# Performance work log

Measured on AMD Instinct MI355X. Metric: run time of the kernel, lower is better.

Reference implementation:

```python
import jax, jax.numpy as jnp
import numpy as np

FREQ_DIM = 32
TIME_DIM = 32
HEADS = 8
TWO_PI = 6.283185307179586


def get_embeddings(B, H, W, freq_dim, time_dim, dtype):
    # freq embeddings over the height (frequency) axis
    nf = freq_dim // 2
    ln_x = jnp.log2(jnp.arange(0, H * nf, dtype=jnp.float32))
    ln_x = ln_x.at[0].set(-2.0)
    ln_x = ln_x.reshape(H, nf).T  # [nf, H]
    ln_x = ln_x * jnp.arange(1, nf + 1, dtype=jnp.float32)[:, None]
    # view_as_real(exp(1j*theta)) -> (cos, sin), interleaved per order along channel dim
    freq = jnp.stack([jnp.cos(ln_x), jnp.sin(ln_x)], axis=1).reshape(freq_dim, H)  # [freq_dim, H]
    freq = jnp.broadcast_to(freq[None, :, :, None], (B, freq_dim, H, W))

    # time embeddings over the width (time) axis
    nt = time_dim // 2
    k = jnp.arange(0, nt, dtype=jnp.float32) + 0.5  # [nt]
    x = jnp.arange(0, nt * W, dtype=jnp.float32).reshape(W, nt).T  # [nt, W]
    theta = k[:, None] * x / (W * nt) * TWO_PI  # [nt, W]
    time = jnp.stack([jnp.cos(theta), jnp.sin(theta)], axis=1).reshape(time_dim, W)  # [time_dim, W]
    time = jnp.broadcast_to(time[None, :, None, :], (B, time_dim, H, W))

    return jnp.concatenate([freq, time], axis=1).astype(dtype)  # [B, freq_dim+time_dim, H, W]


def setup_inputs() -> dict:
    key = jax.random.key(0)
    ks = jax.random.split(key, 6)
    B, C, H, W = 2, 512, 64, 32
    qkC = C + FREQ_DIM + TIME_DIM  # 576
    inner = HEADS * 64  # 512
    return {
        "hidden_states": jax.random.normal(ks[0], (B, C, H, W), dtype=jnp.float32),
        "Wq": jax.random.normal(ks[1], (qkC, inner), dtype=jnp.float32) * 0.02,
        "Wk": jax.random.normal(ks[2], (qkC, inner), dtype=jnp.float32) * 0.02,
        "Wv": jax.random.normal(ks[3], (C, inner), dtype=jnp.float32) * 0.02,
        "Wout": jax.random.normal(ks[4], (inner, C), dtype=jnp.float32) * 0.02,
        "bout": jnp.zeros((C,), dtype=jnp.float32),
    }


def reference(hidden_states, Wq, Wk, Wv, Wout, bout):
    B, C, H, W = hidden_states.shape
    emb = get_embeddings(B, H, W, FREQ_DIM, TIME_DIM, hidden_states.dtype)
    qk_hs = jnp.concatenate([hidden_states, emb], axis=1)  # [B, qkC, H, W]

    S = H * W
    qk_hs = qk_hs.reshape(B, -1, S).transpose(0, 2, 1)  # [B, S, qkC]
    v_hs = hidden_states.reshape(B, C, S).transpose(0, 2, 1)  # [B, S, C]

    q = qk_hs @ Wq  # [B, S, inner]
    k = qk_hs @ Wk
    v = v_hs @ Wv

    hd_qk = q.shape[-1] // HEADS
    hd_v = v.shape[-1] // HEADS
    q = q.reshape(B, S, HEADS, hd_qk).transpose(0, 2, 1, 3)  # [B, h, S, d]
    k = k.reshape(B, S, HEADS, hd_qk).transpose(0, 2, 1, 3)
    v = v.reshape(B, S, HEADS, hd_v).transpose(0, 2, 1, 3)

    scale = 1.0 / jnp.sqrt(jnp.asarray(hd_qk, dtype=q.dtype))
    scores = jnp.einsum('bhqd,bhkd->bhqk', q, k) * scale
    attn = jax.nn.softmax(scores, axis=-1)
    o = jnp.einsum('bhqk,bhkd->bhqd', attn, v)  # [B, h, S, d_v]

    o = o.transpose(0, 2, 1, 3).reshape(B, S, HEADS * hd_v)
    o = o @ Wout + bout  # [B, S, C]
    o = o.transpose(0, 2, 1).reshape(B, C, H, W)

    return o + hidden_states  # residual_connection=True, rescale_output_factor=1.0
```

## Files before the change

kernel.cpp:

```cpp
#include <hip/hip_runtime.h>
#include <math.h>

#define B_    2
#define C_    512
#define H_    64
#define W_    32
#define S_    2048
#define QKC_  576
#define INNER_ 512
#define NH_   8
#define HD_   64
#define TWO_PI_ 6.283185307179586f

typedef __attribute__((ext_vector_type(8))) short bfrag;
typedef __attribute__((ext_vector_type(4))) float ffrag;
typedef __attribute__((ext_vector_type(16))) float f16v;

typedef __attribute__((address_space(1))) const unsigned int as1_u32;
typedef __attribute__((address_space(3))) unsigned int as3_u32;

__device__ __forceinline__ ushort f2bf(float f) {
    unsigned u = __builtin_bit_cast(unsigned, f);
    unsigned r = (u + 0x7FFFu + ((u >> 16) & 1u)) >> 16;
    return (ushort)r;
}

__device__ __forceinline__ f16v zero16() {
    f16v z;
    #pragma unroll
    for (int i = 0; i < 16; i++) z[i] = 0.f;
    return z;
}

#define GLD(gp_, lp_) __builtin_amdgcn_global_load_lds((as1_u32*)(gp_), (as3_u32*)(lp_), 16, 0, 0)
#define EXPA(dst_, x_) asm("v_exp_f32 %0, %1" : "=v"(dst_) : "v"(x_))
#define SC_LOG2E 0.18033688011f

__global__ void k_trans_emb(const float* __restrict__ hid, ushort* __restrict__ X) {
    __shared__ float t[32][33];
    int b  = blockIdx.z;
    int s0 = blockIdx.x * 32, c0 = blockIdx.y * 32;
    int tx = threadIdx.x, ty = threadIdx.y;
    if (c0 < 512) {
        t[ty][tx] = hid[((size_t)b * C_ + (c0 + ty)) * S_ + s0 + tx];
        __syncthreads();
        X[((size_t)(b * S_ + s0 + ty)) * QKC_ + c0 + tx] = f2bf(t[tx][ty]);
    } else {
        int c = c0 - 512 + tx;
        int s = s0 + ty;
        int h = s >> 5, w = s & 31;
        float val;
        if (c < 32) {
            int f = c >> 1;
            int n = h * 16 + f;
            float lx = (n == 0) ? -2.0f : log2f((float)n);
            float arg = lx * (float)(f + 1);
            val = (c & 1) ? sinf(arg) : cosf(arg);
        } else {
            int tt = (c - 32) >> 1;
            float theta = ((float)tt + 0.5f) * (float)(w * 16 + tt) * (TWO_PI_ / 512.0f);
            val = (c & 1) ? sinf(theta) : cosf(theta);
        }
        X[(size_t)(b * S_ + s) * QKC_ + c0 + tx] = f2bf(val);
    }
}

__global__ void k_wtrans_all(const float* __restrict__ Wq, const float* __restrict__ Wk,
                             const float* __restrict__ Wv, const float* __restrict__ Wo,
                             ushort* __restrict__ Wqt, ushort* __restrict__ Wkt,
                             ushort* __restrict__ Wvt, ushort* __restrict__ Wot) {
    __shared__ float t[32][33];
    int z = blockIdx.z;
    const float* W; ushort* Wt; int K;
    if (z == 0)      { W = Wq; Wt = Wqt; K = QKC_; }
    else if (z == 1) { W = Wk; Wt = Wkt; K = QKC_; }
    else if (z == 2) { W = Wv; Wt = Wvt; K = C_; }
    else             { W = Wo; Wt = Wot; K = INNER_; }
    int k0 = blockIdx.x * 32, n0 = blockIdx.y * 32;
    if (k0 >= K) return;
    int tx = threadIdx.x, ty = threadIdx.y;
    t[ty][tx] = W[(size_t)(k0 + ty) * 512 + n0 + tx];
    __syncthreads();
    Wt[(size_t)(n0 + ty) * K + k0 + tx] = f2bf(t[tx][ty]);
}

#define GSTAGE(buf_, k0_) {                                                   \
    _Pragma("unroll")                                                         \
    for (int i_ = 0; i_ < 6; i_++)                                            \
        GLD(gp[i_] + (k0_), tl + (buf_) * 12288 + lo[i_]); }

__global__ __launch_bounds__(256, 3) void k_qkv(const ushort* __restrict__ X,
                                                const ushort* __restrict__ Wqt,
                                                const ushort* __restrict__ Wkt,
                                                const ushort* __restrict__ Wvt,
                                                ushort* __restrict__ Qb,
                                                ushort* __restrict__ Kpk,
                                                ushort* __restrict__ Vpk) {
    __shared__ ushort __attribute__((aligned(16))) tl[2 * 12288];

    int tid = threadIdx.x;
    int l = tid & 63, wv = tid >> 6;
    int wr = wv >> 1, wc = wv & 1;
    int bid = blockIdx.x;
    int lgc = (bid & 7) * 96 + (bid >> 3);
    int bx = lgc % 24, by = lgc / 24;
    int n0 = bx * 64, m0 = by * 128;
    int sel = n0 >> 9, n0l = n0 & 511;
    const ushort* Bt = (sel == 0) ? Wqt : (sel == 1) ? Wkt : Wvt;
    const int K = (sel < 2) ? QKC_ : C_;
    const int nst = K >> 6;
    int l15 = l & 15, lg = l >> 4;
    int swz = l15 & 7;

    const ushort* gp[6];
    unsigned lo[6];
    {
        int rsub = l >> 3;
        int clog = (l & 7) ^ rsub;
        #pragma unroll
        for (int i = 0; i < 6; i++) {
            int c = wv * 6 + i;
            lo[i] = c * 512;
            if (c < 16) gp[i] = X  + (size_t)(m0  + c * 8        + rsub) * QKC_ + clog * 8;
            else        gp[i] = Bt + (size_t)(n0l + (c - 16) * 8 + rsub) * K    + clog * 8;
        }
    }

    ffrag acc[4][2];
    #pragma unroll
    for (int i = 0; i < 4; i++)
        #pragma unroll
        for (int j = 0; j < 2; j++) acc[i][j] = (ffrag){0.f, 0.f, 0.f, 0.f};

    GSTAGE(0, 0);
    int cur = 0;
    for (int kt = 0; kt < nst; kt++) {
        __syncthreads();
        if (kt + 1 < nst) GSTAGE(cur ^ 1, (kt + 1) * 64);
        const ushort* As = tl + cur * 12288;
        const ushort* Bs = As + 8192;
        #pragma unroll
        for (int ks = 0; ks < 2; ks++) {
            int cl = ks * 4 + lg;
            int ch = (cl ^ swz) * 8;
            bfrag af[4], bf[2];
            #pragma unroll
            for (int mi = 0; mi < 4; mi++)
                af[mi] = *(const bfrag*)(As + (wr * 64 + mi * 16 + l15) * 64 + ch);
            #pragma unroll
            for (int nj = 0; nj < 2; nj++)
                bf[nj] = *(const bfrag*)(Bs + (wc * 32 + nj * 16 + l15) * 64 + ch);
            #pragma unroll
            for (int mi = 0; mi < 4; mi++)
                #pragma unroll
                for (int nj = 0; nj < 2; nj++)
                    acc[mi][nj] = __builtin_amdgcn_mfma_f32_16x16x32_bf16(af[mi], bf[nj], acc[mi][nj], 0, 0, 0);
        }
        cur ^= 1;
    }

    if (sel == 0) {
        #pragma unroll
        for (int mi = 0; mi < 4; mi++)
            #pragma unroll
            for (int nj = 0; nj < 2; nj++)
                #pragma unroll
                for (int r = 0; r < 4; r++) {
                    int row = m0 + wr * 64 + mi * 16 + lg * 4 + r;
                    int col = n0l + wc * 32 + nj * 16 + l15;
                    Qb[(size_t)row * INNER_ + col] = f2bf(acc[mi][nj][r]);
                }
    } else {
        ushort (*Ct)[136] = (ushort(*)[136])tl;
        __syncthreads();
        #pragma unroll
        for (int mi = 0; mi < 4; mi++)
            #pragma unroll
            for (int nj = 0; nj < 2; nj++)
                #pragma unroll
                for (int r = 0; r < 4; r++)
                    Ct[wc * 32 + nj * 16 + l15][wr * 64 + mi * 16 + lg * 4 + r] = f2bf(acc[mi][nj][r]);
        __syncthreads();
        int pair = (m0 >> 11) * 8 + (n0l >> 6);
        int kvb0 = (m0 & 2047) >> 5;
        if (sel == 1) {
            #pragma unroll
            for (int p = 0; p < 4; p++) {
                int cid = tid + p * 256;
                int sl = cid >> 7, kv = cid & 127;
                bfrag tmp;
                #pragma unroll
                for (int j = 0; j < 8; j++) tmp[j] = (short)Ct[sl * 8 + j][kv];
                ushort* dst = Kpk + ((size_t)((pair * 64 + kvb0 + (kv >> 5)) * 8 + sl)) * 256 + (kv & 31) * 8;
                *(uint4*)dst = __builtin_bit_cast(uint4, tmp);
            }
        } else {
            #pragma unroll
            for (int p = 0; p < 4; p++) {
                int cid = tid + p * 256;
                int d = cid >> 4, mc = cid & 15;
                uint4 v = *(uint4*)&Ct[d][mc * 8];
                ushort* dst = Vpk + ((size_t)((pair * 64 + kvb0 + (mc >> 2)) * 4 + (mc & 3))) * 512 + d * 8;
                *(uint4*)dst = v;
            }
        }
    }
}

__global__ __launch_bounds__(256, 2) void k_og(const ushort* __restrict__ Ob,
                                               const ushort* __restrict__ Wot,
                                               const float* __restrict__ bias,
                                               const float* __restrict__ hid,
                                               float* __restrict__ out) {
    __shared__ ushort __attribute__((aligned(16))) tl[2 * 12288];

    int tid = threadIdx.x;
    int l = tid & 63, wv = tid >> 6;
    int wr = wv >> 1, wc = wv & 1;
    int bid = blockIdx.x;
    int lgc = (bid & 7) * 32 + (bid >> 3);
    int bx = lgc & 7, by = lgc >> 3;
    int n0 = bx * 64, m0 = by * 128;
    int l15 = l & 15, lg = l >> 4;
    int swz = l15 & 7;

    const ushort* gp[6];
    unsigned lo[6];
    {
        int rsub = l >> 3;
        int clog = (l & 7) ^ rsub;
        #pragma unroll
        for (int i = 0; i < 6; i++) {
            int c = wv * 6 + i;
            lo[i] = c * 512;
            if (c < 16) gp[i] = Ob  + (size_t)(m0 + c * 8        + rsub) * INNER_ + clog * 8;
            else        gp[i] = Wot + (size_t)(n0 + (c - 16) * 8 + rsub) * INNER_ + clog * 8;
        }
    }

    ffrag acc[4][2];
    #pragma unroll
    for (int i = 0; i < 4; i++)
        #pragma unroll
        for (int j = 0; j < 2; j++) acc[i][j] = (ffrag){0.f, 0.f, 0.f, 0.f};

    GSTAGE(0, 0);
    int cur = 0;
    for (int kt = 0; kt < 8; kt++) {
        __syncthreads();
        if (kt < 7) GSTAGE(cur ^ 1, (kt + 1) * 64);
        const ushort* As = tl + cur * 12288;
        const ushort* Bs = As + 8192;
        #pragma unroll
        for (int ks = 0; ks < 2; ks++) {
            int cl = ks * 4 + lg;
            int ch = (cl ^ swz) * 8;
            bfrag af[4], bf[2];
            #pragma unroll
            for (int mi = 0; mi < 4; mi++)
                af[mi] = *(const bfrag*)(As + (wr * 64 + mi * 16 + l15) * 64 + ch);
            #pragma unroll
            for (int nj = 0; nj < 2; nj++)
                bf[nj] = *(const bfrag*)(Bs + (wc * 32 + nj * 16 + l15) * 64 + ch);
            #pragma unroll
            for (int mi = 0; mi < 4; mi++)
                #pragma unroll
                for (int nj = 0; nj < 2; nj++)
                    acc[mi][nj] = __builtin_amdgcn_mfma_f32_16x16x32_bf16(af[mi], bf[nj], acc[mi][nj], 0, 0, 0);
        }
        cur ^= 1;
    }

    float (*Cf)[129] = (float(*)[129])tl;
    float bv[2];
    #pragma unroll
    for (int nj = 0; nj < 2; nj++) bv[nj] = bias[n0 + wc * 32 + nj * 16 + l15];
    __syncthreads();
    #pragma unroll
    for (int mi = 0; mi < 4; mi++)
        #pragma unroll
        for (int nj = 0; nj < 2; nj++)
            #pragma unroll
            for (int r = 0; r < 4; r++)
                Cf[wc * 32 + nj * 16 + l15][wr * 64 + mi * 16 + lg * 4 + r] = acc[mi][nj][r] + bv[nj];
    __syncthreads();
    int b = m0 >> 11, s0m = m0 & 2047;
    #pragma unroll
    for (int p = 0; p < 8; p++) {
        int f = p * 256 + tid;
        int c = f >> 5, sq = (f & 31) * 4;
        size_t o = (((size_t)(b * 512 + n0 + c)) << 11) + s0m + sq;
        float4 hv = *(const float4*)(hid + o);
        float4 cv = *(float4*)&Cf[c][sq];
        cv.x += hv.x; cv.y += hv.y; cv.z += hv.z; cv.w += hv.w;
        *(float4*)(out + o) = cv;
    }
}

#define CVTPK(dst, a, b) asm("v_cvt_pk_bf16_f32 %0, %1, %2" : "=v"(dst) : "v"(a), "v"(b))
#define SWAP32(a, b)     asm("v_permlane32_swap_b32 %0, %1" : "+v"(a), "+v"(b))

#define ASTAGE(buf_, kt_) {                                                   \
    const ushort* g_ = (qg ? vpb : kpb) + (size_t)(kt_) * 2048 + l * 8;       \
    ushort* lp_ = ktv + spb + (buf_) * 4096 + (qg ? 2048 : 0);                \
    _Pragma("unroll")                                                         \
    for (int i_ = 0; i_ < 4; i_++)                                            \
        GLD(g_ + i_ * 512, lp_ + i_ * 512); }

__global__ __launch_bounds__(512, 4) void k_attn(const ushort* __restrict__ Qf,
                                                 const ushort* __restrict__ Kpk,
                                                 const ushort* __restrict__ Vpk,
                                                 ushort* __restrict__ Ob) {
    __shared__ __attribute__((aligned(16))) char smem[69632];
    ushort* ktv = (ushort*)smem;
    float*  cmb = (float*)smem;
    float*  mlsh = (float*)(smem + 67584);

    const int id = blockIdx.x;
    const int lgc = (id & 7) * 64 + (id >> 3);
    const int qb = lgc & 31, pair = lgc >> 5;
    const int hd = pair & 7, b = pair >> 3;

    const int tid = threadIdx.x;
    const int l = tid & 63, wv = tid >> 6;
    const int qg = wv >> 2, sp = wv & 3;
    const int l31 = l & 31, hi = l >> 5;
    const int hoff = hd * HD_;
    const int brow = b * S_ + qb * 64;

    bfrag qf[4];
    {
        const ushort* qp = Qf + (size_t)(brow + qg * 32 + l31) * INNER_ + hoff + hi * 8;
        #pragma unroll
        for (int ks = 0; ks < 4; ks++) qf[ks] = *(const bfrag*)(qp + ks * 16);
    }

    const ushort* kpb = Kpk + ((size_t)pair * 64 + sp * 16) * 2048;
    const ushort* vpb = Vpk + ((size_t)pair * 64 + sp * 16) * 2048;
    const int spb  = sp * 8192;
    const int koff = l31 * 8 + hi * 256;
    const int voff = l31 * 8 + hi * 512;

    ASTAGE(0, 0);

    float m_run = -INFINITY, l_run = 0.f;
    f16v acc0 = zero16(), acc1 = zero16();
    int buf = 0;

    for (int kt = 0; kt < 16; kt++) {
        __syncthreads();
        if (kt < 15) ASTAGE(buf ^ 1, kt + 1);

        const ushort* Kt = ktv + spb + buf * 4096;
        const ushort* Vt = Kt + 2048;

        f16v sf0 = zero16();
        #pragma unroll
        for (int ks = 0; ks < 4; ks++) {
            bfrag kfr = *(const bfrag*)(Kt + ks * 512 + koff);
            sf0 = __builtin_amdgcn_mfma_f32_32x32x16_bf16(kfr, qf[ks], sf0, 0, 0, 0);
        }

        float t8[8];
        #pragma unroll
        for (int j = 0; j < 8; j++) t8[j] = fmaxf(sf0[j], sf0[j + 8]);
        float t4a = fmaxf(t8[0], t8[4]), t4b = fmaxf(t8[1], t8[5]);
        float t4c = fmaxf(t8[2], t8[6]), t4d = fmaxf(t8[3], t8[7]);
        float tm = fmaxf(fmaxf(t4a, t4b), fmaxf(t4c, t4d));
        tm = fmaxf(tm, __shfl_xor(tm, 32));
        if (!__all(tm <= m_run + 64.0f)) {
            float mn = fmaxf(m_run, tm);
            float corr; EXPA(corr, (m_run - mn) * SC_LOG2E);
            l_run *= corr;
            #pragma unroll
            for (int j = 0; j < 16; j++) { acc0[j] *= corr; acc1[j] *= corr; }
            m_run = mn;
        }
        float nm = -m_run * SC_LOG2E;
        #pragma unroll
        for (int j = 0; j < 16; j++) { float p; EXPA(p, fmaf(sf0[j], SC_LOG2E, nm)); sf0[j] = p; }
        float s8[8];
        #pragma unroll
        for (int j = 0; j < 8; j++) s8[j] = sf0[j] + sf0[j + 8];
        float ls = ((s8[0] + s8[4]) + (s8[1] + s8[5])) + ((s8[2] + s8[6]) + (s8[3] + s8[7]));
        ls += __shfl_xor(ls, 32);
        l_run += ls;

        #pragma unroll
        for (int s = 0; s < 2; s++) {
            unsigned A0, B0, A1, B1;
            CVTPK(A0, sf0[s * 8 + 0], sf0[s * 8 + 1]); CVTPK(B0, sf0[s * 8 + 4], sf0[s * 8 + 5]);
            SWAP32(A0, B0);
            CVTPK(A1, sf0[s * 8 + 2], sf0[s * 8 + 3]); CVTPK(B1, sf0[s * 8 + 6], sf0[s * 8 + 7]);
            SWAP32(A1, B1);
            uint4 u; u.x = A0; u.y = A1; u.z = B0; u.w = B1;
            bfrag pa = __builtin_bit_cast(bfrag, u);
            bfrag v0 = *(const bfrag*)(Vt + s * 1024 + voff);
            bfrag v1 = *(const bfrag*)(Vt + s * 1024 + voff + 256);
            acc0 = __builtin_amdgcn_mfma_f32_32x32x16_bf16(v0, pa, acc0, 0, 0, 0);
            acc1 = __builtin_amdgcn_mfma_f32_32x32x16_bf16(v1, pa, acc1, 0, 0, 0);
        }

        buf ^= 1;
    }

    if (hi == 0) {
        mlsh[(qg * 4 + sp) * 64 + l31]      = m_run;
        mlsh[(qg * 4 + sp) * 64 + 32 + l31] = l_run;
    }
    __syncthreads();
    {
        float* creg = cmb + (qg * 4 + sp) * 2112;
        #pragma unroll
        for (int j = 0; j < 16; j++) {
            int d0 = (j & 3) + 8 * (j >> 2) + 4 * hi;
            creg[d0 * 33 + l31]        = acc0[j];
            creg[(d0 + 32) * 33 + l31] = acc1[j];
        }
    }
    __syncthreads();
    {
        int qgE = tid >> 8;
        int t2 = tid & 255;
        int qq = t2 >> 3, cc = t2 & 7;
        float mh[4], lh[4], cs[4];
        float mg = -INFINITY;
        #pragma unroll
        for (int h = 0; h < 4; h++) {
            mh[h] = mlsh[(qgE * 4 + h) * 64 + qq];
            lh[h] = mlsh[(qgE * 4 + h) * 64 + 32 + qq];
            mg = fmaxf(mg, mh[h]);
        }
        float tot = 0.f;
        #pragma unroll
        for (int h = 0; h < 4; h++) { EXPA(cs[h], (mh[h] - mg) * SC_LOG2E); tot += cs[h] * lh[h]; }
        float inv = 1.0f / tot;
        bfrag ov;
        #pragma unroll
        for (int j = 0; j < 8; j++) {
            int d = cc * 8 + j;
            float s = 0.f;
            #pragma unroll
            for (int h = 0; h < 4; h++) s += cs[h] * cmb[(qgE * 4 + h) * 2112 + d * 33 + qq];
            ov[j] = (short)f2bf(s * inv);
        }
        *(uint4*)(Ob + (size_t)(brow + qgE * 32 + qq) * INNER_ + hoff + cc * 8) = __builtin_bit_cast(uint4, ov);
    }
}

extern "C" void kernel_launch(void* const* d_in, const int* in_sizes, int n_in,
                              void* d_out, int out_size, void* d_ws, size_t ws_size,
                              hipStream_t stream) {
    const float* hid  = (const float*)d_in[0];
    const float* Wq   = (const float*)d_in[1];
    const float* Wk   = (const float*)d_in[2];
    const float* Wv   = (const float*)d_in[3];
    const float* Wout = (const float*)d_in[4];
    const float* bout = (const float*)d_in[5];
    float* out = (float*)d_out;

    const int M = B_ * S_;
    char* w = (char*)d_ws;
    ushort* X    = (ushort*)w;                    w += (size_t)M * QKC_ * 2;
    ushort* Qb   = (ushort*)w;                    w += (size_t)M * INNER_ * 2;
    ushort* Kpk  = (ushort*)w;                    w += (size_t)M * INNER_ * 2;
    ushort* Vpk  = (ushort*)w;                    w += (size_t)M * INNER_ * 2;
    ushort* Ob   = (ushort*)w;                    w += (size_t)M * INNER_ * 2;
    ushort* Wqt  = (ushort*)w;                    w += (size_t)INNER_ * QKC_ * 2;
    ushort* Wkt  = (ushort*)w;                    w += (size_t)INNER_ * QKC_ * 2;
    ushort* Wvt  = (ushort*)w;                    w += (size_t)INNER_ * C_ * 2;
    ushort* Wot  = (ushort*)w;                    w += (size_t)C_ * INNER_ * 2;

    k_wtrans_all<<<dim3(18, 16, 4), dim3(32, 32), 0, stream>>>(Wq, Wk, Wv, Wout,
                                                               Wqt, Wkt, Wvt, Wot);
    k_trans_emb<<<dim3(S_ / 32, 18, B_), dim3(32, 32), 0, stream>>>(hid, X);

    k_qkv<<<dim3(768), 256, 0, stream>>>(X, Wqt, Wkt, Wvt, Qb, Kpk, Vpk);

    k_attn<<<dim3(512), 512, 0, stream>>>(Qb, Kpk, Vpk, Ob);

    k_og<<<dim3(256), 256, 0, stream>>>(Ob, Wot, bout, hid, out);
}
```

Before: 66.80 us.

## Restructure attention with per-wave private K/V staging and 128-row query tiles

Attention blocks now cover 128 query rows with 8 waves, arranged as 4 query groups by 2 key splits, and the grid halves to 256 blocks. Each wave streams its own K and V tiles into a private double-buffered LDS region, synchronised with waitcnt instead of block-wide barriers. MFMA sections are wrapped in s_setprio, and the XCD-aware block mapping is changed. This removes per-iteration __syncthreads, but it uses twice the shared memory, lowers blocks per CU, halves the split-K parallelism, and gives fewer blocks to fill 256 CUs.

Result: slower. 72.83 us (+9.0%).

```diff
diff --git a/kernel.cpp b/kernel.cpp
--- a/kernel.cpp
+++ b/kernel.cpp
@@ -301,43 +301,46 @@
 #define SWAP32(a, b)     asm("v_permlane32_swap_b32 %0, %1" : "+v"(a), "+v"(b))
 
 #define ASTAGE(buf_, kt_) {                                                   \
-    const ushort* g_ = (qg ? vpb : kpb) + (size_t)(kt_) * 2048 + l * 8;       \
-    ushort* lp_ = ktv + spb + (buf_) * 4096 + (qg ? 2048 : 0);                \
+    const ushort* gk_ = kpb + (size_t)(kt_) * 2048 + l * 8;                   \
+    const ushort* gv_ = vpb + (size_t)(kt_) * 2048 + l * 8;                   \
+    ushort* lk_ = lbase + (buf_) * 4096;                                      \
     _Pragma("unroll")                                                         \
-    for (int i_ = 0; i_ < 4; i_++)                                            \
-        GLD(g_ + i_ * 512, lp_ + i_ * 512); }
-
-__global__ __launch_bounds__(512, 4) void k_attn(const ushort* __restrict__ Qf,
+    for (int i_ = 0; i_ < 4; i_++) GLD(gk_ + i_ * 512, lk_ + i_ * 512);       \
+    _Pragma("unroll")                                                         \
+    for (int i_ = 0; i_ < 4; i_++) GLD(gv_ + i_ * 512, lk_ + 2048 + i_ * 512); }
+
+__global__ __launch_bounds__(512, 2) void k_attn(const ushort* __restrict__ Qf,
                                                  const ushort* __restrict__ Kpk,
                                                  const ushort* __restrict__ Vpk,
                                                  ushort* __restrict__ Ob) {
-    __shared__ __attribute__((aligned(16))) char smem[69632];
-    ushort* ktv = (ushort*)smem;
-    float*  cmb = (float*)smem;
-    float*  mlsh = (float*)(smem + 67584);
-
-    const int id = blockIdx.x;
-    const int lgc = (id & 7) * 64 + (id >> 3);
-    const int qb = lgc & 31, pair = lgc >> 5;
+    __shared__ __attribute__((aligned(16))) char smem[133120];
+    ushort* ktv  = (ushort*)smem;
+    float*  cmb  = (float*)smem;
+    float*  mlsh = (float*)(smem + 131072);
+
+    const int id  = blockIdx.x;
+    const int xcd = id & 7, wi = id >> 3;
+    const int pair = xcd * 2 + (wi >> 4);
+    const int qt   = wi & 15;
     const int hd = pair & 7, b = pair >> 3;
 
     const int tid = threadIdx.x;
-    const int l = tid & 63, wv = tid >> 6;
-    const int qg = wv >> 2, sp = wv & 3;
+    const int l = tid & 63, wvid = tid >> 6;
+    const int qi = wvid >> 1, sp = wvid & 1;
     const int l31 = l & 31, hi = l >> 5;
     const int hoff = hd * HD_;
-    const int brow = b * S_ + qb * 64;
+    const int brow = b * S_ + qt * 128;
 
     bfrag qf[4];
     {
-        const ushort* qp = Qf + (size_t)(brow + qg * 32 + l31) * INNER_ + hoff + hi * 8;
+        const ushort* qp = Qf + (size_t)(brow + qi * 32 + l31) * INNER_ + hoff + hi * 8;
         #pragma unroll
         for (int ks = 0; ks < 4; ks++) qf[ks] = *(const bfrag*)(qp + ks * 16);
     }
 
-    const ushort* kpb = Kpk + ((size_t)pair * 64 + sp * 16) * 2048;
-    const ushort* vpb = Vpk + ((size_t)pair * 64 + sp * 16) * 2048;
-    const int spb  = sp * 8192;
+    const ushort* kpb = Kpk + ((size_t)pair * 64 + sp * 32) * 2048;
+    const ushort* vpb = Vpk + ((size_t)pair * 64 + sp * 32) * 2048;
+    ushort* lbase = ktv + wvid * 8192;
     const int koff = l31 * 8 + hi * 256;
     const int voff = l31 * 8 + hi * 512;
 
@@ -347,19 +350,27 @@
     f16v acc0 = zero16(), acc1 = zero16();
     int buf = 0;
 
-    for (int kt = 0; kt < 16; kt++) {
-        __syncthreads();
-        if (kt < 15) ASTAGE(buf ^ 1, kt + 1);
-
-        const ushort* Kt = ktv + spb + buf * 4096;
+    for (int kt = 0; kt < 32; kt++) {
+        if (kt < 31) {
+            asm volatile("s_waitcnt lgkmcnt(0)" ::: "memory");
+            ASTAGE(buf ^ 1, kt + 1);
+            asm volatile("s_waitcnt vmcnt(8)" ::: "memory");
+        } else {
+            asm volatile("s_waitcnt vmcnt(0)" ::: "memory");
+        }
+        __builtin_amdgcn_sched_barrier(0);
+
+        const ushort* Kt = lbase + buf * 4096;
         const ushort* Vt = Kt + 2048;
 
         f16v sf0 = zero16();
+        __builtin_amdgcn_s_setprio(1);
         #pragma unroll
         for (int ks = 0; ks < 4; ks++) {
             bfrag kfr = *(const bfrag*)(Kt + ks * 512 + koff);
             sf0 = __builtin_amdgcn_mfma_f32_32x32x16_bf16(kfr, qf[ks], sf0, 0, 0, 0);
         }
+        __builtin_amdgcn_s_setprio(0);
 
         float t8[8];
         #pragma unroll
@@ -386,6 +397,7 @@
         ls += __shfl_xor(ls, 32);
         l_run += ls;
 
+        __builtin_amdgcn_s_setprio(1);
         #pragma unroll
         for (int s = 0; s < 2; s++) {
             unsigned A0, B0, A1, B1;
@@ -400,17 +412,18 @@
             acc0 = __builtin_amdgcn_mfma_f32_32x32x16_bf16(v0, pa, acc0, 0, 0, 0);
             acc1 = __builtin_amdgcn_mfma_f32_32x32x16_bf16(v1, pa, acc1, 0, 0, 0);
         }
+        __builtin_amdgcn_s_setprio(0);
 
         buf ^= 1;
     }
 
     if (hi == 0) {
-        mlsh[(qg * 4 + sp) * 64 + l31]      = m_run;
-        mlsh[(qg * 4 + sp) * 64 + 32 + l31] = l_run;
+        mlsh[wvid * 64 + l31]      = m_run;
+        mlsh[wvid * 64 + 32 + l31] = l_run;
     }
     __syncthreads();
     {
-        float* creg = cmb + (qg * 4 + sp) * 2112;
+        float* creg = cmb + wvid * 2112;
         #pragma unroll
         for (int j = 0; j < 16; j++) {
             int d0 = (j & 3) + 8 * (j >> 2) + 4 * hi;
@@ -419,21 +432,23 @@
         }
     }
     __syncthreads();
-    {
-        int qgE = tid >> 8;
-        int t2 = tid & 255;
+    #pragma unroll
+    for (int p2 = 0; p2 < 2; p2++) {
+        int f = p2 * 512 + tid;
+        int qg4 = f >> 8;
+        int t2 = f & 255;
         int qq = t2 >> 3, cc = t2 & 7;
-        float mh[4], lh[4], cs[4];
+        float mh[2], lh[2], cs[2];
         float mg = -INFINITY;
         #pragma unroll
-        for (int h = 0; h < 4; h++) {
-            mh[h] = mlsh[(qgE * 4 + h) * 64 + qq];
-            lh[h] = mlsh[(qgE * 4 + h) * 64 + 32 + qq];
+        for (int h = 0; h < 2; h++) {
+            mh[h] = mlsh[(qg4 * 2 + h) * 64 + qq];
+            lh[h] = mlsh[(qg4 * 2 + h) * 64 + 32 + qq];
             mg = fmaxf(mg, mh[h]);
         }
         float tot = 0.f;
         #pragma unroll
-        for (int h = 0; h < 4; h++) { EXPA(cs[h], (mh[h] - mg) * SC_LOG2E); tot += cs[h] * lh[h]; }
+        for (int h = 0; h < 2; h++) { EXPA(cs[h], (mh[h] - mg) * SC_LOG2E); tot += cs[h] * lh[h]; }
         float inv = 1.0f / tot;
         bfrag ov;
         #pragma unroll
@@ -441,10 +456,10 @@
             int d = cc * 8 + j;
             float s = 0.f;
             #pragma unroll
-            for (int h = 0; h < 4; h++) s += cs[h] * cmb[(qgE * 4 + h) * 2112 + d * 33 + qq];
+            for (int h = 0; h < 2; h++) s += cs[h] * cmb[(qg4 * 2 + h) * 2112 + d * 33 + qq];
             ov[j] = (short)f2bf(s * inv);
         }
-        *(uint4*)(Ob + (size_t)(brow + qgE * 32 + qq) * INNER_ + hoff + cc * 8) = __builtin_bit_cast(uint4, ov);
+        *(uint4*)(Ob + (size_t)(brow + qg4 * 32 + qq) * INNER_ + hoff + cc * 8) = __builtin_bit_cast(uint4, ov);
     }
 }
 
@@ -477,7 +492,7 @@
 
     k_qkv<<<dim3(768), 256, 0, stream>>>(X, Wqt, Wkt, Wvt, Qb, Kpk, Vpk);
 
-    k_attn<<<dim3(512), 512, 0, stream>>>(Qb, Kpk, Vpk, Ob);
+    k_attn<<<dim3(256), 512, 0, stream>>>(Qb, Kpk, Vpk, Ob);
 
     k_og<<<dim3(256), 256, 0, stream>>>(Ob, Wot, bout, hid, out);
 }
```
